# Performance work log

Measured on AMD Instinct MI355X. Metric: run time of the kernel, lower is better.

Reference implementation:

```python
import jax, jax.numpy as jnp
from jax import lax
import numpy as np

B, T, C, HID, H, W = 8, 24, 3, 32, 64, 64


def setup_inputs() -> dict:
    key = jax.random.key(0)
    ks = jax.random.split(key, 8)
    def n(k, shape, s=0.05):
        return jax.random.normal(k, shape, dtype=jnp.float32) * s
    return {
        "x": n(ks[0], (B, T, C, H, W), 1.0),
        # encoder layer 0: conv over concat(x, h) -> 4*HID gate channels
        "Wenc0": n(ks[1], (4 * HID, C + HID, 3, 3)),
        "benc0": jnp.zeros((4 * HID,), jnp.float32),
        # encoder layer 1: input is layer-0 hidden seq (HID channels)
        "Wenc1": n(ks[2], (4 * HID, HID + HID, 3, 3)),
        "benc1": jnp.zeros((4 * HID,), jnp.float32),
        # decoder (1 layer, input_dim channels in)
        "Wdec": n(ks[3], (4 * HID, C + HID, 3, 3)),
        "bdec": jnp.zeros((4 * HID,), jnp.float32),
        # MLP head: HID*H*W -> 256 -> 97
        "fc1_w": n(ks[4], (256, HID * H * W), 0.01),
        "fc1_b": jnp.zeros((256,), jnp.float32),
        "fc2_w": n(ks[5], (97, 256)),
        "fc2_b": jnp.zeros((97,), jnp.float32),
    }


def _cell_step(h, c, x_t, Wk, b):
    # ConvLSTM cell: conv(concat(x,h)) -> i,f,o,g gates
    z = lax.conv_general_dilated(
        jnp.concatenate([x_t, h], axis=1), Wk,
        window_strides=(1, 1), padding='SAME',
        dimension_numbers=('NCHW', 'OIHW', 'NCHW')) + b[None, :, None, None]
    i, f, o, g = jnp.split(z, 4, axis=1)
    c_new = jax.nn.sigmoid(f) * c + jax.nn.sigmoid(i) * jnp.tanh(g)
    h_new = jax.nn.sigmoid(o) * jnp.tanh(c_new)
    return h_new, c_new


def _run_layer(x_tb, Wk, b):
    # x_tb: [T, B, Cin, H, W]; zero-initialized state
    h0 = jnp.zeros((x_tb.shape[1], HID, H, W), x_tb.dtype)
    c0 = jnp.zeros_like(h0)
    def step(hc, xt):
        h, c = _cell_step(hc[0], hc[1], xt, Wk, b)
        return (h, c), h
    (hT, cT), hs = lax.scan(step, (h0, c0), x_tb)
    return hs, (hT, cT)


def reference(x, Wenc0, benc0, Wenc1, benc1, Wdec, bdec, fc1_w, fc1_b, fc2_w, fc2_b):
    x_tb = jnp.transpose(x, (1, 0, 2, 3, 4))          # [T,B,C,H,W]
    hs0, _ = _run_layer(x_tb, Wenc0, benc0)           # layer-0 hidden seq
    _, (hT, cT) = _run_layer(hs0, Wenc1, benc1)       # last-layer final state
    # decoder: one step on last input frame, seeded with encoder state
    h_dec, _ = _cell_step(hT, cT, x[:, -1], Wdec, bdec)  # [B,HID,H,W]
    feat = h_dec.reshape(h_dec.shape[0], -1)          # [B, HID*H*W]
    hdn = jax.nn.relu(feat @ fc1_w.T + fc1_b)
    return hdn @ fc2_w.T + fc2_b                      # [B, 97]
```

## Files before the change

kernel.cpp:

```cpp
#include <hip/hip_runtime.h>

typedef __attribute__((ext_vector_type(8))) short short8v;
typedef __attribute__((ext_vector_type(4))) float f32x4;
typedef __attribute__((ext_vector_type(4))) unsigned int uint4v;
typedef unsigned short u16;

__device__ __forceinline__ u16 f2bf(float f) {
  unsigned u = __float_as_uint(f);
  u += 0x7FFFu + ((u >> 16) & 1u);
  return (u16)(u >> 16);
}
__device__ __forceinline__ short8v ld8(const u16* p) {
  return *reinterpret_cast<const short8v*>(p);
}
__device__ __forceinline__ float frcp(float x) { return __builtin_amdgcn_rcpf(x); }

__device__ __forceinline__ void st_cg(u16* p, uint4v v) {
  asm volatile("global_store_dwordx4 %0, %1, off sc0 sc1" :: "v"(p), "v"(v) : "memory");
}
__device__ __forceinline__ void ld2_cg(const u16* a0, const u16* a1,
                                       uint4v& v0, uint4v& v1) {
  asm volatile(
      "global_load_dwordx4 %0, %2, off sc0 sc1\n\t"
      "global_load_dwordx4 %1, %3, off sc0 sc1\n\t"
      "s_waitcnt vmcnt(0)"
      : "=&v"(v0), "=&v"(v1) : "v"(a0), "v"(a1) : "memory");
}
__device__ __forceinline__ void ld4_cg(const u16* a0, const u16* a1, const u16* a2,
                                       const u16* a3, uint4v& v0, uint4v& v1,
                                       uint4v& v2, uint4v& v3) {
  asm volatile(
      "global_load_dwordx4 %0, %4, off sc0 sc1\n\t"
      "global_load_dwordx4 %1, %5, off sc0 sc1\n\t"
      "global_load_dwordx4 %2, %6, off sc0 sc1\n\t"
      "global_load_dwordx4 %3, %7, off sc0 sc1\n\t"
      "s_waitcnt vmcnt(0)"
      : "=&v"(v0), "=&v"(v1), "=&v"(v2), "=&v"(v3)
      : "v"(a0), "v"(a1), "v"(a2), "v"(a3)
      : "memory");
}

__device__ __forceinline__ void poll_lane(const unsigned* a, unsigned tgt, bool active) {
  bool pending = active;
  while (__ballot(pending)) {
    if (pending &&
        __hip_atomic_load((unsigned*)a, __ATOMIC_RELAXED, __HIP_MEMORY_SCOPE_AGENT) >= tgt)
      pending = false;
    if (__ballot(pending)) __builtin_amdgcn_s_sleep(1);
  }
}
__device__ __forceinline__ void publish(unsigned* f, unsigned v) {
  __syncthreads();
  if (threadIdx.x == 0)
    __hip_atomic_store(f, v, __ATOMIC_RELAXED, __HIP_MEMORY_SCOPE_AGENT);
}

__global__ void k_pack(const float* __restrict__ We0, const float* __restrict__ We1,
                       const float* __restrict__ Wd,
                       u16* __restrict__ Wh0p, u16* __restrict__ Wx1p,
                       u16* __restrict__ Wh1p, u16* __restrict__ Whdp,
                       u16* __restrict__ Wx0p, u16* __restrict__ Wxdp,
                       unsigned* __restrict__ flags) {
  int i = blockIdx.x * 256 + threadIdx.x;
  if (i < 8192) flags[i] = 0u;
  if (i < 147456) {
    int tbl = i / 36864, j = i % 36864;
    int s = j >> 12, cg = (j >> 11) & 1, gate = (j >> 9) & 3,
        chl = (j >> 5) & 15, ci = j & 31;
    int co = gate * 32 + cg * 16 + chl;
    float v;
    if (tbl == 0)      v = We0[(co * 35 + 3 + ci) * 9 + s];
    else if (tbl == 1) v = We1[(co * 64 + ci) * 9 + s];
    else if (tbl == 2) v = We1[(co * 64 + 32 + ci) * 9 + s];
    else               v = Wd[(co * 35 + 3 + ci) * 9 + s];
    u16* dst = tbl == 0 ? Wh0p : tbl == 1 ? Wx1p : tbl == 2 ? Wh1p : Whdp;
    dst[j] = f2bf(v);
  } else {
    int j = i - 147456, tbl = j >> 12;
    j &= 4095;
    int cg = (j >> 11) & 1, gate = (j >> 9) & 3, chl = (j >> 5) & 15, k = j & 31;
    int co = gate * 32 + cg * 16 + chl;
    const float* src = tbl ? Wd : We0;
    u16 v = (k < 27) ? f2bf(src[(co * 35 + (k % 3)) * 9 + (k / 3)]) : (u16)0;
    (tbl ? Wxdp : Wx0p)[j] = v;
  }
}

__global__ void k_im2col(const float* __restrict__ x, u16* __restrict__ out) {
  int p = blockIdx.x * 256 + threadIdx.x;
  int t = p >> 15;
  int rem = p & 32767;
  int b = rem >> 12;
  int yy = (rem >> 6) & 63;
  int xx = rem & 63;
  __align__(16) u16 buf[32];
#pragma unroll
  for (int k = 27; k < 32; k++) buf[k] = 0;
  const float* xb = x + ((size_t)(b * 24 + t)) * 3 * 4096;
#pragma unroll
  for (int ky = 0; ky < 3; ky++) {
    int ys = yy + ky - 1;
    bool yok = (unsigned)ys < 64u;
#pragma unroll
    for (int kx = 0; kx < 3; kx++) {
      int xs = xx + kx - 1;
      bool ok = yok && ((unsigned)xs < 64u);
#pragma unroll
      for (int ci = 0; ci < 3; ci++) {
        float v = ok ? xb[(size_t)ci * 4096 + ys * 64 + xs] : 0.f;
        buf[(ky * 3 + kx) * 3 + ci] = f2bf(v);
      }
    }
  }
  uint4v* dst = (uint4v*)(out + (size_t)p * 32);
  const uint4v* s = (const uint4v*)buf;
  dst[0] = s[0]; dst[1] = s[1]; dst[2] = s[2]; dst[3] = s[3];
}

__global__ __launch_bounds__(256, 1) void k_persist(
    const u16* __restrict__ imc, u16* __restrict__ hs0G, u16* __restrict__ h1G,
    const u16* __restrict__ Wx0, const u16* __restrict__ Wh0,
    const float* __restrict__ be0,
    const u16* __restrict__ Wx1, const u16* __restrict__ Wh1,
    const float* __restrict__ be1,
    const u16* __restrict__ Wxd, const u16* __restrict__ Whd,
    const float* __restrict__ bd,
    float* __restrict__ hdec, unsigned* __restrict__ flag) {
  __shared__ __align__(16) u16 smH0[8448];
  __shared__ __align__(16) u16 smH1[8448];
  const int bid = blockIdx.x;
  const int b = bid & 7;
  const int yblk = bid >> 3;
  const int y0 = yblk << 1;
  const int fi = bid * 16;
  const int tid = threadIdx.x;
  const int l = tid & 63, w = tid >> 6, lr = l & 15, g = l >> 4;
  const int mh = w >> 1, cg = w & 1, y = y0 + mh;

  if (tid < 64) {
    int q = tid & 31;
    int rgq = q >> 1, side = q & 1;
    u16* base = (tid < 32 ? smH0 : smH1) + ((size_t)(rgq * 66 + side * 65)) * 8;
    *(uint4v*)base = (uint4v)0u;
  }

  const int ch = cg * 16 + lr;
  const float bI0 = be0[ch], bF0 = be0[32 + ch], bO0 = be0[64 + ch], bG0 = be0[96 + ch];
  const float bI1 = be1[ch], bF1 = be1[32 + ch], bO1 = be1[64 + ch], bG1 = be1[96 + ch];
  const float bId = bd[ch],  bFd = bd[32 + ch],  bOd = bd[64 + ch],  bGd = bd[96 + ch];
  float c0r[16], c1r[16];
#pragma unroll
  for (int i = 0; i < 16; i++) { c0r[i] = 0.f; c1r[i] = 0.f; }

  const int pxs = tid >> 2, gqs = tid & 3;
  const size_t rbG = (size_t)b * 131072;
  const size_t poff = (size_t)pxs * 32 + gqs * 8;
  const int rup = (yblk == 0) ? y0 : y0 - 1;
  const int rdn = (yblk == 31) ? y0 + 1 : y0 + 2;
  u16* dUp0 = smH0 + ((size_t)(gqs * 66 + pxs + 1)) * 8;
  u16* dDn0 = smH0 + ((size_t)((12 + gqs) * 66 + pxs + 1)) * 8;
  u16* dUp1 = smH1 + ((size_t)(gqs * 66 + pxs + 1)) * 8;
  u16* dDn1 = smH1 + ((size_t)((12 + gqs) * 66 + pxs + 1)) * 8;

  auto do_shifts = [&](const u16* sm, const u16* __restrict__ W, f32x4 (&acc)[4][4]) {
#pragma unroll
    for (int sft = 0; sft < 9; sft++) {
      const int ky = sft / 3, dx = sft % 3 - 1;
      const u16* wb = W + ((size_t)(sft * 2 + cg) * 64 + lr) * 32 + g * 8;
      short8v B0 = ld8(wb), B1 = ld8(wb + 512), B2 = ld8(wb + 1024), B3 = ld8(wb + 1536);
      const u16* abase = sm + ((size_t)(((mh + ky) * 4 + g) * 66 + lr + dx + 1)) * 8;
#pragma unroll
      for (int mt = 0; mt < 4; mt++) {
        short8v A = ld8(abase + mt * 128);
        acc[mt][0] = __builtin_amdgcn_mfma_f32_16x16x32_bf16(A, B0, acc[mt][0], 0, 0, 0);
        acc[mt][1] = __builtin_amdgcn_mfma_f32_16x16x32_bf16(A, B1, acc[mt][1], 0, 0, 0);
        acc[mt][2] = __builtin_amdgcn_mfma_f32_16x16x32_bf16(A, B2, acc[mt][2], 0, 0, 0);
        acc[mt][3] = __builtin_amdgcn_mfma_f32_16x16x32_bf16(A, B3, acc[mt][3], 0, 0, 0);
      }
    }
  };
  auto imcol = [&](const u16* xp, const u16* __restrict__ W, f32x4 (&acc)[4][4]) {
    const u16* ab = xp + rbG + (size_t)y * 2048 + g * 8;
    const u16* wb = W + (cg * 64 + lr) * 32 + g * 8;
    short8v B0 = ld8(wb), B1 = ld8(wb + 512), B2 = ld8(wb + 1024), B3 = ld8(wb + 1536);
#pragma unroll
    for (int mt = 0; mt < 4; mt++) {
      short8v A = ld8(ab + (mt * 16 + lr) * 32);
      acc[mt][0] = __builtin_amdgcn_mfma_f32_16x16x32_bf16(A, B0, acc[mt][0], 0, 0, 0);
      acc[mt][1] = __builtin_amdgcn_mfma_f32_16x16x32_bf16(A, B1, acc[mt][1], 0, 0, 0);
      acc[mt][2] = __builtin_amdgcn_mfma_f32_16x16x32_bf16(A, B2, acc[mt][2], 0, 0, 0);
      acc[mt][3] = __builtin_amdgcn_mfma_f32_16x16x32_bf16(A, B3, acc[mt][3], 0, 0, 0);
    }
  };
  auto gates = [&](f32x4 (&acc)[4][4], float* cr, float bI, float bF, float bO,
                   float bG, u16* hbf) {
#pragma unroll
    for (int mt = 0; mt < 4; mt++) {
#pragma unroll
      for (int j = 0; j < 4; j++) {
        float zi = acc[mt][0][j] + bI, zf = acc[mt][1][j] + bF;
        float zo = acc[mt][2][j] + bO, zg = acc[mt][3][j] + bG;
        float ei = __expf(-zi), ef = __expf(-zf), eo = __expf(-zo);
        float eg = __expf(2.f * zg);
        float cn = frcp(1.f + ef) * cr[mt * 4 + j] +
                   (eg - 1.f) * frcp((1.f + ei) * (eg + 1.f));
        float ec = __expf(2.f * cn);
        cr[mt * 4 + j] = cn;
        hbf[mt * 4 + j] = f2bf((ec - 1.f) * frcp((1.f + eo) * (ec + 1.f)));
      }
    }
  };

  for (int s = 0; s <= 25; ++s) {
    if (s > 0 && tid < 64) {
      const unsigned* a = nullptr; bool act = false;
      if (l == 0 && yblk > 0)  { a = flag + fi - 128; act = true; }
      if (l == 1 && yblk < 31) { a = flag + fi + 128; act = true; }
      poll_lane(a, (unsigned)s, act);
    }
    __syncthreads();

    const bool st0 = (s >= 1 && s <= 24);
    const bool st1 = (s >= 2);
    if (st0 || st1) {
      const u16* h0src = hs0G + (size_t)((s - 1) & 1) * 1048576 + rbG;
      const u16* h1src = h1G + (size_t)(s & 1) * 1048576 + rbG;
      uint4v v0 = (uint4v)0u, v1 = (uint4v)0u, v2 = (uint4v)0u, v3 = (uint4v)0u;
      if (st0 && st1)
        ld4_cg(h0src + (size_t)rup * 2048 + poff, h0src + (size_t)rdn * 2048 + poff,
               h1src + (size_t)rup * 2048 + poff, h1src + (size_t)rdn * 2048 + poff,
               v0, v1, v2, v3);
      else if (st0)
        ld2_cg(h0src + (size_t)rup * 2048 + poff, h0src + (size_t)rdn * 2048 + poff,
               v0, v1);
      else
        ld2_cg(h1src + (size_t)rup * 2048 + poff, h1src + (size_t)rdn * 2048 + poff,
               v2, v3);
      if (yblk == 0)  { v0 = (uint4v)0u; v2 = (uint4v)0u; }
      if (yblk == 31) { v1 = (uint4v)0u; v3 = (uint4v)0u; }
      if (st0) { *(uint4v*)dUp0 = v0; *(uint4v*)dDn0 = v1; }
      if (st1) { *(uint4v*)dUp1 = v2; *(uint4v*)dDn1 = v3; }
    }
    __syncthreads();

    const bool doL0 = (s <= 23);
    const bool doL1 = (s >= 1 && s <= 24);
    u16 hbf0[16], hbf1[16];

    if (doL0) {
      f32x4 acc[4][4];
#pragma unroll
      for (int i = 0; i < 4; i++)
#pragma unroll
        for (int j = 0; j < 4; j++) acc[i][j] = (f32x4)0.f;
      imcol(imc + (size_t)s * 1048576, Wx0, acc);
      if (s >= 1) do_shifts(smH0, Wh0, acc);
      gates(acc, c0r, bI0, bF0, bO0, bG0, hbf0);
    }
    if (doL1) {
      f32x4 acc[4][4];
#pragma unroll
      for (int i = 0; i < 4; i++)
#pragma unroll
        for (int j = 0; j < 4; j++) acc[i][j] = (f32x4)0.f;
      do_shifts(smH0, Wx1, acc);
      if (s >= 2) do_shifts(smH1, Wh1, acc);
      gates(acc, c1r, bI1, bF1, bO1, bG1, hbf1);
    }
    if (s == 25) {
      f32x4 acc[4][4];
#pragma unroll
      for (int i = 0; i < 4; i++)
#pragma unroll
        for (int j = 0; j < 4; j++) acc[i][j] = (f32x4)0.f;
      imcol(imc + (size_t)23 * 1048576, Wxd, acc);
      do_shifts(smH1, Whd, acc);
#pragma unroll
      for (int mt = 0; mt < 4; mt++) {
#pragma unroll
        for (int j = 0; j < 4; j++) {
          int px = mt * 16 + g * 4 + j;
          float zi = acc[mt][0][j] + bId, zf = acc[mt][1][j] + bFd;
          float zo = acc[mt][2][j] + bOd, zg = acc[mt][3][j] + bGd;
          float ei = __expf(-zi), ef = __expf(-zf), eo = __expf(-zo);
          float eg = __expf(2.f * zg);
          float cn = frcp(1.f + ef) * c1r[mt * 4 + j] +
                     (eg - 1.f) * frcp((1.f + ei) * (eg + 1.f));
          float ec = __expf(2.f * cn);
          float hn = (ec - 1.f) * frcp((1.f + eo) * (ec + 1.f));
          hdec[((size_t)(b * 32 + ch) * 64 + y) * 64 + px] = hn;
        }
      }
      return;
    }
    __syncthreads();

    if (doL0) {
#pragma unroll
      for (int mt = 0; mt < 4; mt++)
#pragma unroll
        for (int j = 0; j < 4; j++) {
          int px = mt * 16 + g * 4 + j;
          smH0[((size_t)((1 + mh) * 4 + (ch >> 3)) * 66 + px + 1) * 8 + (ch & 7)] =
              hbf0[mt * 4 + j];
        }
    }
    if (doL1) {
#pragma unroll
      for (int mt = 0; mt < 4; mt++)
#pragma unroll
        for (int j = 0; j < 4; j++) {
          int px = mt * 16 + g * 4 + j;
          smH1[((size_t)((1 + mh) * 4 + (ch >> 3)) * 66 + px + 1) * 8 + (ch & 7)] =
              hbf1[mt * 4 + j];
        }
    }
    __syncthreads();

    if (doL0) {
      u16* d = hs0G + (size_t)(s & 1) * 1048576 + rbG;
      st_cg(d + (size_t)y0 * 2048 + poff,
            *(const uint4v*)(smH0 + ((size_t)(4 + gqs) * 66 + pxs + 1) * 8));
      st_cg(d + (size_t)(y0 + 1) * 2048 + poff,
            *(const uint4v*)(smH0 + ((size_t)(8 + gqs) * 66 + pxs + 1) * 8));
    }
    if (doL1) {
      u16* d = h1G + (size_t)((s - 1) & 1) * 1048576 + rbG;
      st_cg(d + (size_t)y0 * 2048 + poff,
            *(const uint4v*)(smH1 + ((size_t)(4 + gqs) * 66 + pxs + 1) * 8));
      st_cg(d + (size_t)(y0 + 1) * 2048 + poff,
            *(const uint4v*)(smH1 + ((size_t)(8 + gqs) * 66 + pxs + 1) * 8));
    }
    publish(flag + fi, (unsigned)(s + 1));
  }
}

__global__ __launch_bounds__(256) void k_fc1(const float* __restrict__ w,
                                             const float* __restrict__ feat,
                                             float* __restrict__ partial) {
  __shared__ float fsm[8][1024];
  const int ng = blockIdx.x, ks = blockIdx.y;
  const int tid = threadIdx.x;
  const float* fb = feat + (size_t)ks * 1024;
  for (int i = tid; i < 2048; i += 256) {
    int bb = i >> 8, kk = (i & 255) << 2;
    *(f32x4*)&fsm[bb][kk] = *(const f32x4*)(fb + (size_t)bb * 131072 + kk);
  }
  __syncthreads();
  const int wv = tid >> 6, lane = tid & 63;
  const int n0 = ng * 16 + wv * 4;
  const float* wr = w + (size_t)n0 * 131072 + (size_t)ks * 1024;
  float acc[4][8];
#pragma unroll
  for (int i = 0; i < 4; i++)
#pragma unroll
    for (int j = 0; j < 8; j++) acc[i][j] = 0.f;
#pragma unroll
  for (int it = 0; it < 4; it++) {
    int k = it * 256 + lane * 4;
    f32x4 w0 = *(const f32x4*)(wr + k);
    f32x4 w1 = *(const f32x4*)(wr + 131072 + k);
    f32x4 w2 = *(const f32x4*)(wr + 262144 + k);
    f32x4 w3 = *(const f32x4*)(wr + 393216 + k);
#pragma unroll
    for (int bb = 0; bb < 8; bb++) {
      f32x4 fv = *(const f32x4*)&fsm[bb][k];
      acc[0][bb] += w0[0] * fv[0] + w0[1] * fv[1] + w0[2] * fv[2] + w0[3] * fv[3];
      acc[1][bb] += w1[0] * fv[0] + w1[1] * fv[1] + w1[2] * fv[2] + w1[3] * fv[3];
      acc[2][bb] += w2[0] * fv[0] + w2[1] * fv[1] + w2[2] * fv[2] + w2[3] * fv[3];
      acc[3][bb] += w3[0] * fv[0] + w3[1] * fv[1] + w3[2] * fv[2] + w3[3] * fv[3];
    }
  }
#pragma unroll
  for (int nn = 0; nn < 4; nn++)
#pragma unroll
    for (int bb = 0; bb < 8; bb++) {
      float v = acc[nn][bb];
#pragma unroll
      for (int m = 32; m >= 1; m >>= 1) v += __shfl_xor(v, m, 64);
      if (lane == 0) partial[((size_t)ks * 8 + bb) * 256 + n0 + nn] = v;
    }
}

__global__ void k_fc1_fin(const float* __restrict__ partial,
                          const float* __restrict__ b1, float* __restrict__ hdn) {
  int i = blockIdx.x * 256 + threadIdx.x;
  if (i >= 2048) return;
  int b = i >> 8, n = i & 255;
  float v = b1[n];
  for (int ks = 0; ks < 128; ks++) v += partial[((size_t)ks * 8 + b) * 256 + n];
  hdn[i] = fmaxf(v, 0.f);
}

__global__ void k_fc2(const float* __restrict__ hdn, const float* __restrict__ w2,
                      const float* __restrict__ b2, float* __restrict__ out) {
  int i = blockIdx.x * 256 + threadIdx.x;
  if (i >= 776) return;
  int b = i / 97, m = i % 97;
  const float* h = hdn + b * 256;
  const float* wr = w2 + m * 256;
  float v = b2[m];
  for (int k = 0; k < 256; k++) v += h[k] * wr[k];
  out[i] = v;
}

extern "C" void kernel_launch(void* const* d_in, const int* in_sizes, int n_in,
                              void* d_out, int out_size, void* d_ws, size_t ws_size,
                              hipStream_t stream) {
  const float* x   = (const float*)d_in[0];
  const float* We0 = (const float*)d_in[1];
  const float* be0 = (const float*)d_in[2];
  const float* We1 = (const float*)d_in[3];
  const float* be1 = (const float*)d_in[4];
  const float* Wd  = (const float*)d_in[5];
  const float* bd  = (const float*)d_in[6];
  const float* f1w = (const float*)d_in[7];
  const float* f1b = (const float*)d_in[8];
  const float* f2w = (const float*)d_in[9];
  const float* f2b = (const float*)d_in[10];

  char* ws = (char*)d_ws;
  u16*      imc  = (u16*)(ws + 0);
  u16*      hs0G = (u16*)(ws + 50331648);
  u16*      h1G  = (u16*)(ws + 54525952);
  u16*      wp   = (u16*)(ws + 58720256);
  float*    hdec = (float*)(ws + 62914560);
  unsigned* flag = (unsigned*)(ws + 67108864);
  float*    part = (float*)(ws + 0);
  float*    hdn  = (float*)(ws + 1048576);
  u16 *Wh0p = wp, *Wx1p = wp + 36864, *Wh1p = wp + 73728, *Whdp = wp + 110592,
      *Wx0p = wp + 147456, *Wxdp = wp + 151552;

  k_pack<<<608, 256, 0, stream>>>(We0, We1, Wd, Wh0p, Wx1p, Wh1p, Whdp, Wx0p,
                                  Wxdp, flag);
  k_im2col<<<3072, 256, 0, stream>>>(x, imc);

  k_persist<<<256, 256, 0, stream>>>(imc, hs0G, h1G, Wx0p, Wh0p, be0,
                                     Wx1p, Wh1p, be1, Wxdp, Whdp, bd, hdec, flag);

  k_fc1<<<dim3(16, 128), 256, 0, stream>>>(f1w, hdec, part);
  k_fc1_fin<<<8, 256, 0, stream>>>(part, f1b, hdn);
  k_fc2<<<4, 256, 0, stream>>>(hdn, f2w, f2b, (float*)d_out);
}
```

Measured before the change: 375.4 us.

## Split layer-0 and layer-1 work across separate wave groups in persistent kernel

The persistent ConvLSTM kernel goes from 256 to 512 threads per block. Waves 0-3 compute encoder layer 0 and waves 4-7 compute layer 1, where before the same waves ran both layers one after the other. Each half also loads and stores its own halo rows, and each thread keeps a single cell-state array. This is meant to run the two layers' MFMA work concurrently and reduce per-thread register pressure, at the cost of larger blocks and an extra barrier per step.

```diff
diff --git a/kernel.cpp b/kernel.cpp
--- a/kernel.cpp
+++ b/kernel.cpp
@@ -25,19 +25,6 @@
       "global_load_dwordx4 %1, %3, off sc0 sc1\n\t"
       "s_waitcnt vmcnt(0)"
       : "=&v"(v0), "=&v"(v1) : "v"(a0), "v"(a1) : "memory");
-}
-__device__ __forceinline__ void ld4_cg(const u16* a0, const u16* a1, const u16* a2,
-                                       const u16* a3, uint4v& v0, uint4v& v1,
-                                       uint4v& v2, uint4v& v3) {
-  asm volatile(
-      "global_load_dwordx4 %0, %4, off sc0 sc1\n\t"
-      "global_load_dwordx4 %1, %5, off sc0 sc1\n\t"
-      "global_load_dwordx4 %2, %6, off sc0 sc1\n\t"
-      "global_load_dwordx4 %3, %7, off sc0 sc1\n\t"
-      "s_waitcnt vmcnt(0)"
-      : "=&v"(v0), "=&v"(v1), "=&v"(v2), "=&v"(v3)
-      : "v"(a0), "v"(a1), "v"(a2), "v"(a3)
-      : "memory");
 }
 
 __device__ __forceinline__ void poll_lane(const unsigned* a, unsigned tgt, bool active) {
@@ -117,7 +104,7 @@
   dst[0] = s[0]; dst[1] = s[1]; dst[2] = s[2]; dst[3] = s[3];
 }
 
-__global__ __launch_bounds__(256, 1) void k_persist(
+__global__ __launch_bounds__(512, 1) void k_persist(
     const u16* __restrict__ imc, u16* __restrict__ hs0G, u16* __restrict__ h1G,
     const u16* __restrict__ Wx0, const u16* __restrict__ Wh0,
     const float* __restrict__ be0,
@@ -134,8 +121,10 @@
   const int y0 = yblk << 1;
   const int fi = bid * 16;
   const int tid = threadIdx.x;
-  const int l = tid & 63, w = tid >> 6, lr = l & 15, g = l >> 4;
-  const int mh = w >> 1, cg = w & 1, y = y0 + mh;
+  const int w = tid >> 6, l = tid & 63, lr = l & 15, g = l >> 4;
+  const bool isL1w = w >= 4;
+  const int lw = w & 3, mh = lw >> 1, cg = lw & 1, y = y0 + mh;
+  const int ch = cg * 16 + lr;
 
   if (tid < 64) {
     int q = tid & 31;
@@ -144,23 +133,22 @@
     *(uint4v*)base = (uint4v)0u;
   }
 
-  const int ch = cg * 16 + lr;
-  const float bI0 = be0[ch], bF0 = be0[32 + ch], bO0 = be0[64 + ch], bG0 = be0[96 + ch];
-  const float bI1 = be1[ch], bF1 = be1[32 + ch], bO1 = be1[64 + ch], bG1 = be1[96 + ch];
-  const float bId = bd[ch],  bFd = bd[32 + ch],  bOd = bd[64 + ch],  bGd = bd[96 + ch];
-  float c0r[16], c1r[16];
-#pragma unroll
-  for (int i = 0; i < 16; i++) { c0r[i] = 0.f; c1r[i] = 0.f; }
-
-  const int pxs = tid >> 2, gqs = tid & 3;
+  const float* bia = isL1w ? be1 : be0;
+  const float bI = bia[ch], bF = bia[32 + ch], bO = bia[64 + ch], bG = bia[96 + ch];
+  float cr[16];
+#pragma unroll
+  for (int i = 0; i < 16; i++) cr[i] = 0.f;
+
+  const int sthr = tid & 255;
+  const int sgrp = tid >> 8;
+  const int pxs = sthr >> 2, gqs = sthr & 3;
   const size_t rbG = (size_t)b * 131072;
   const size_t poff = (size_t)pxs * 32 + gqs * 8;
   const int rup = (yblk == 0) ? y0 : y0 - 1;
   const int rdn = (yblk == 31) ? y0 + 1 : y0 + 2;
-  u16* dUp0 = smH0 + ((size_t)(gqs * 66 + pxs + 1)) * 8;
-  u16* dDn0 = smH0 + ((size_t)((12 + gqs) * 66 + pxs + 1)) * 8;
-  u16* dUp1 = smH1 + ((size_t)(gqs * 66 + pxs + 1)) * 8;
-  u16* dDn1 = smH1 + ((size_t)((12 + gqs) * 66 + pxs + 1)) * 8;
+  u16* smS = sgrp ? smH1 : smH0;
+  u16* dUp = smS + ((size_t)(gqs * 66 + pxs + 1)) * 8;
+  u16* dDn = smS + ((size_t)((12 + gqs) * 66 + pxs + 1)) * 8;
 
   auto do_shifts = [&](const u16* sm, const u16* __restrict__ W, f32x4 (&acc)[4][4]) {
 #pragma unroll
@@ -192,8 +180,7 @@
       acc[mt][3] = __builtin_amdgcn_mfma_f32_16x16x32_bf16(A, B3, acc[mt][3], 0, 0, 0);
     }
   };
-  auto gates = [&](f32x4 (&acc)[4][4], float* cr, float bI, float bF, float bO,
-                   float bG, u16* hbf) {
+  auto gates = [&](f32x4 (&acc)[4][4], u16* hbf) {
 #pragma unroll
     for (int mt = 0; mt < 4; mt++) {
 #pragma unroll
@@ -220,32 +207,57 @@
     }
     __syncthreads();
 
-    const bool st0 = (s >= 1 && s <= 24);
-    const bool st1 = (s >= 2);
-    if (st0 || st1) {
-      const u16* h0src = hs0G + (size_t)((s - 1) & 1) * 1048576 + rbG;
-      const u16* h1src = h1G + (size_t)(s & 1) * 1048576 + rbG;
-      uint4v v0 = (uint4v)0u, v1 = (uint4v)0u, v2 = (uint4v)0u, v3 = (uint4v)0u;
-      if (st0 && st1)
-        ld4_cg(h0src + (size_t)rup * 2048 + poff, h0src + (size_t)rdn * 2048 + poff,
-               h1src + (size_t)rup * 2048 + poff, h1src + (size_t)rdn * 2048 + poff,
-               v0, v1, v2, v3);
-      else if (st0)
-        ld2_cg(h0src + (size_t)rup * 2048 + poff, h0src + (size_t)rdn * 2048 + poff,
-               v0, v1);
-      else
-        ld2_cg(h1src + (size_t)rup * 2048 + poff, h1src + (size_t)rdn * 2048 + poff,
-               v2, v3);
-      if (yblk == 0)  { v0 = (uint4v)0u; v2 = (uint4v)0u; }
-      if (yblk == 31) { v1 = (uint4v)0u; v3 = (uint4v)0u; }
-      if (st0) { *(uint4v*)dUp0 = v0; *(uint4v*)dDn0 = v1; }
-      if (st1) { *(uint4v*)dUp1 = v2; *(uint4v*)dDn1 = v3; }
+    if (sgrp == 0 && s >= 1 && s <= 24) {
+      const u16* src = hs0G + (size_t)((s - 1) & 1) * 1048576 + rbG;
+      uint4v v0, v1;
+      ld2_cg(src + (size_t)rup * 2048 + poff, src + (size_t)rdn * 2048 + poff, v0, v1);
+      if (yblk == 0)  v0 = (uint4v)0u;
+      if (yblk == 31) v1 = (uint4v)0u;
+      *(uint4v*)dUp = v0; *(uint4v*)dDn = v1;
+    }
+    if (sgrp == 1 && s >= 2) {
+      const u16* src = h1G + (size_t)(s & 1) * 1048576 + rbG;
+      uint4v v0, v1;
+      ld2_cg(src + (size_t)rup * 2048 + poff, src + (size_t)rdn * 2048 + poff, v0, v1);
+      if (yblk == 0)  v0 = (uint4v)0u;
+      if (yblk == 31) v1 = (uint4v)0u;
+      *(uint4v*)dUp = v0; *(uint4v*)dDn = v1;
     }
     __syncthreads();
 
-    const bool doL0 = (s <= 23);
-    const bool doL1 = (s >= 1 && s <= 24);
-    u16 hbf0[16], hbf1[16];
+    if (s == 25) {
+      if (isL1w) {
+        f32x4 acc[4][4];
+#pragma unroll
+        for (int i = 0; i < 4; i++)
+#pragma unroll
+          for (int j = 0; j < 4; j++) acc[i][j] = (f32x4)0.f;
+        imcol(imc + (size_t)23 * 1048576, Wxd, acc);
+        do_shifts(smH1, Whd, acc);
+        const float bId = bd[ch], bFd = bd[32 + ch], bOd = bd[64 + ch], bGd = bd[96 + ch];
+#pragma unroll
+        for (int mt = 0; mt < 4; mt++) {
+#pragma unroll
+          for (int j = 0; j < 4; j++) {
+            int px = mt * 16 + g * 4 + j;
+            float zi = acc[mt][0][j] + bId, zf = acc[mt][1][j] + bFd;
+            float zo = acc[mt][2][j] + bOd, zg = acc[mt][3][j] + bGd;
+            float ei = __expf(-zi), ef = __expf(-zf), eo = __expf(-zo);
+            float eg = __expf(2.f * zg);
+            float cn = frcp(1.f + ef) * cr[mt * 4 + j] +
+                       (eg - 1.f) * frcp((1.f + ei) * (eg + 1.f));
+            float ec = __expf(2.f * cn);
+            float hn = (ec - 1.f) * frcp((1.f + eo) * (ec + 1.f));
+            hdec[((size_t)(b * 32 + ch) * 64 + y) * 64 + px] = hn;
+          }
+        }
+      }
+      return;
+    }
+
+    const bool doL0 = !isL1w && s <= 23;
+    const bool doL1 = isL1w && s >= 1 && s <= 24;
+    u16 hbf[16];
 
     if (doL0) {
       f32x4 acc[4][4];
@@ -255,7 +267,7 @@
         for (int j = 0; j < 4; j++) acc[i][j] = (f32x4)0.f;
       imcol(imc + (size_t)s * 1048576, Wx0, acc);
       if (s >= 1) do_shifts(smH0, Wh0, acc);
-      gates(acc, c0r, bI0, bF0, bO0, bG0, hbf0);
+      gates(acc, hbf);
     }
     if (doL1) {
       f32x4 acc[4][4];
@@ -265,66 +277,31 @@
         for (int j = 0; j < 4; j++) acc[i][j] = (f32x4)0.f;
       do_shifts(smH0, Wx1, acc);
       if (s >= 2) do_shifts(smH1, Wh1, acc);
-      gates(acc, c1r, bI1, bF1, bO1, bG1, hbf1);
-    }
-    if (s == 25) {
-      f32x4 acc[4][4];
-#pragma unroll
-      for (int i = 0; i < 4; i++)
-#pragma unroll
-        for (int j = 0; j < 4; j++) acc[i][j] = (f32x4)0.f;
-      imcol(imc + (size_t)23 * 1048576, Wxd, acc);
-      do_shifts(smH1, Whd, acc);
-#pragma unroll
-      for (int mt = 0; mt < 4; mt++) {
+      gates(acc, hbf);
+    }
+    __syncthreads();
+
+    if (doL0 || doL1) {
+      u16* smD = isL1w ? smH1 : smH0;
+#pragma unroll
+      for (int mt = 0; mt < 4; mt++)
 #pragma unroll
         for (int j = 0; j < 4; j++) {
           int px = mt * 16 + g * 4 + j;
-          float zi = acc[mt][0][j] + bId, zf = acc[mt][1][j] + bFd;
-          float zo = acc[mt][2][j] + bOd, zg = acc[mt][3][j] + bGd;
-          float ei = __expf(-zi), ef = __expf(-zf), eo = __expf(-zo);
-          float eg = __expf(2.f * zg);
-          float cn = frcp(1.f + ef) * c1r[mt * 4 + j] +
-                     (eg - 1.f) * frcp((1.f + ei) * (eg + 1.f));
-          float ec = __expf(2.f * cn);
-          float hn = (ec - 1.f) * frcp((1.f + eo) * (ec + 1.f));
-          hdec[((size_t)(b * 32 + ch) * 64 + y) * 64 + px] = hn;
+          smD[((size_t)((1 + mh) * 4 + (ch >> 3)) * 66 + px + 1) * 8 + (ch & 7)] =
+              hbf[mt * 4 + j];
         }
-      }
-      return;
     }
     __syncthreads();
 
-    if (doL0) {
-#pragma unroll
-      for (int mt = 0; mt < 4; mt++)
-#pragma unroll
-        for (int j = 0; j < 4; j++) {
-          int px = mt * 16 + g * 4 + j;
-          smH0[((size_t)((1 + mh) * 4 + (ch >> 3)) * 66 + px + 1) * 8 + (ch & 7)] =
-              hbf0[mt * 4 + j];
-        }
-    }
-    if (doL1) {
-#pragma unroll
-      for (int mt = 0; mt < 4; mt++)
-#pragma unroll
-        for (int j = 0; j < 4; j++) {
-          int px = mt * 16 + g * 4 + j;
-          smH1[((size_t)((1 + mh) * 4 + (ch >> 3)) * 66 + px + 1) * 8 + (ch & 7)] =
-              hbf1[mt * 4 + j];
-        }
-    }
-    __syncthreads();
-
-    if (doL0) {
+    if (sgrp == 0 && s <= 23) {
       u16* d = hs0G + (size_t)(s & 1) * 1048576 + rbG;
       st_cg(d + (size_t)y0 * 2048 + poff,
             *(const uint4v*)(smH0 + ((size_t)(4 + gqs) * 66 + pxs + 1) * 8));
       st_cg(d + (size_t)(y0 + 1) * 2048 + poff,
             *(const uint4v*)(smH0 + ((size_t)(8 + gqs) * 66 + pxs + 1) * 8));
     }
-    if (doL1) {
+    if (sgrp == 1 && s >= 1 && s <= 24) {
       u16* d = h1G + (size_t)((s - 1) & 1) * 1048576 + rbG;
       st_cg(d + (size_t)y0 * 2048 + poff,
             *(const uint4v*)(smH1 + ((size_t)(4 + gqs) * 66 + pxs + 1) * 8));
@@ -435,7 +412,7 @@
                                   Wxdp, flag);
   k_im2col<<<3072, 256, 0, stream>>>(x, imc);
 
-  k_persist<<<256, 256, 0, stream>>>(imc, hs0G, h1G, Wx0p, Wh0p, be0,
+  k_persist<<<256, 512, 0, stream>>>(imc, hs0G, h1G, Wx0p, Wh0p, be0,
                                      Wx1p, Wh1p, be1, Wxdp, Whdp, bd, hdec, flag);
 
   k_fc1<<<dim3(16, 128), 256, 0, stream>>>(f1w, hdec, part);
```

Result: faster. 337.1 us (-10.2%).

## Split persistent ConvLSTM into one-row blocks with layer-specialized waves

Applied to the files above, without the earlier changes.

The persistent recurrent kernel now launches 512 blocks of one image row each instead of 256 blocks of two rows. Within a block, waves 0-1 compute encoder layer 0 and waves 2-3 compute layer 1 (and the decoder step), where before every wave ran both layers in sequence. Launch bounds now request two blocks per CU. The goal is to shorten the serial per-timestep critical path and raise occupancy, at the cost of twice as many neighbour-flag syncs and halo loads, and an uneven load between the layer-0 and layer-1 waves.

```diff
diff --git a/kernel.cpp b/kernel.cpp
--- a/kernel.cpp
+++ b/kernel.cpp
@@ -117,7 +117,7 @@
   dst[0] = s[0]; dst[1] = s[1]; dst[2] = s[2]; dst[3] = s[3];
 }
 
-__global__ __launch_bounds__(256, 1) void k_persist(
+__global__ __launch_bounds__(256, 2) void k_persist(
     const u16* __restrict__ imc, u16* __restrict__ hs0G, u16* __restrict__ h1G,
     const u16* __restrict__ Wx0, const u16* __restrict__ Wh0,
     const float* __restrict__ be0,
@@ -126,41 +126,41 @@
     const u16* __restrict__ Wxd, const u16* __restrict__ Whd,
     const float* __restrict__ bd,
     float* __restrict__ hdec, unsigned* __restrict__ flag) {
-  __shared__ __align__(16) u16 smH0[8448];
-  __shared__ __align__(16) u16 smH1[8448];
+  __shared__ __align__(16) u16 smH0[6336];
+  __shared__ __align__(16) u16 smH1[6336];
   const int bid = blockIdx.x;
   const int b = bid & 7;
   const int yblk = bid >> 3;
-  const int y0 = yblk << 1;
+  const int y0 = yblk;
   const int fi = bid * 16;
   const int tid = threadIdx.x;
-  const int l = tid & 63, w = tid >> 6, lr = l & 15, g = l >> 4;
-  const int mh = w >> 1, cg = w & 1, y = y0 + mh;
-
-  if (tid < 64) {
-    int q = tid & 31;
+  const int w = tid >> 6, l = tid & 63, lr = l & 15, g = l >> 4;
+  const bool isL1w = w >= 2;
+  const int cg = w & 1;
+  const int ch = cg * 16 + lr;
+
+  if (tid < 48) {
+    int op = tid / 24, q = tid % 24;
     int rgq = q >> 1, side = q & 1;
-    u16* base = (tid < 32 ? smH0 : smH1) + ((size_t)(rgq * 66 + side * 65)) * 8;
+    u16* base = (op ? smH1 : smH0) + ((size_t)(rgq * 66 + side * 65)) * 8;
     *(uint4v*)base = (uint4v)0u;
   }
 
-  const int ch = cg * 16 + lr;
-  const float bI0 = be0[ch], bF0 = be0[32 + ch], bO0 = be0[64 + ch], bG0 = be0[96 + ch];
-  const float bI1 = be1[ch], bF1 = be1[32 + ch], bO1 = be1[64 + ch], bG1 = be1[96 + ch];
-  const float bId = bd[ch],  bFd = bd[32 + ch],  bOd = bd[64 + ch],  bGd = bd[96 + ch];
-  float c0r[16], c1r[16];
-#pragma unroll
-  for (int i = 0; i < 16; i++) { c0r[i] = 0.f; c1r[i] = 0.f; }
+  const float* bia = isL1w ? be1 : be0;
+  const float bI = bia[ch], bF = bia[32 + ch], bO = bia[64 + ch], bG = bia[96 + ch];
+  float cr[16];
+#pragma unroll
+  for (int i = 0; i < 16; i++) cr[i] = 0.f;
 
   const int pxs = tid >> 2, gqs = tid & 3;
   const size_t rbG = (size_t)b * 131072;
   const size_t poff = (size_t)pxs * 32 + gqs * 8;
   const int rup = (yblk == 0) ? y0 : y0 - 1;
-  const int rdn = (yblk == 31) ? y0 + 1 : y0 + 2;
+  const int rdn = (yblk == 63) ? y0 : y0 + 1;
   u16* dUp0 = smH0 + ((size_t)(gqs * 66 + pxs + 1)) * 8;
-  u16* dDn0 = smH0 + ((size_t)((12 + gqs) * 66 + pxs + 1)) * 8;
+  u16* dDn0 = smH0 + ((size_t)((8 + gqs) * 66 + pxs + 1)) * 8;
   u16* dUp1 = smH1 + ((size_t)(gqs * 66 + pxs + 1)) * 8;
-  u16* dDn1 = smH1 + ((size_t)((12 + gqs) * 66 + pxs + 1)) * 8;
+  u16* dDn1 = smH1 + ((size_t)((8 + gqs) * 66 + pxs + 1)) * 8;
 
   auto do_shifts = [&](const u16* sm, const u16* __restrict__ W, f32x4 (&acc)[4][4]) {
 #pragma unroll
@@ -168,7 +168,7 @@
       const int ky = sft / 3, dx = sft % 3 - 1;
       const u16* wb = W + ((size_t)(sft * 2 + cg) * 64 + lr) * 32 + g * 8;
       short8v B0 = ld8(wb), B1 = ld8(wb + 512), B2 = ld8(wb + 1024), B3 = ld8(wb + 1536);
-      const u16* abase = sm + ((size_t)(((mh + ky) * 4 + g) * 66 + lr + dx + 1)) * 8;
+      const u16* abase = sm + ((size_t)((ky * 4 + g) * 66 + lr + dx + 1)) * 8;
 #pragma unroll
       for (int mt = 0; mt < 4; mt++) {
         short8v A = ld8(abase + mt * 128);
@@ -180,7 +180,7 @@
     }
   };
   auto imcol = [&](const u16* xp, const u16* __restrict__ W, f32x4 (&acc)[4][4]) {
-    const u16* ab = xp + rbG + (size_t)y * 2048 + g * 8;
+    const u16* ab = xp + rbG + (size_t)y0 * 2048 + g * 8;
     const u16* wb = W + (cg * 64 + lr) * 32 + g * 8;
     short8v B0 = ld8(wb), B1 = ld8(wb + 512), B2 = ld8(wb + 1024), B3 = ld8(wb + 1536);
 #pragma unroll
@@ -192,8 +192,7 @@
       acc[mt][3] = __builtin_amdgcn_mfma_f32_16x16x32_bf16(A, B3, acc[mt][3], 0, 0, 0);
     }
   };
-  auto gates = [&](f32x4 (&acc)[4][4], float* cr, float bI, float bF, float bO,
-                   float bG, u16* hbf) {
+  auto gates = [&](f32x4 (&acc)[4][4], u16* hbf) {
 #pragma unroll
     for (int mt = 0; mt < 4; mt++) {
 #pragma unroll
@@ -215,7 +214,7 @@
     if (s > 0 && tid < 64) {
       const unsigned* a = nullptr; bool act = false;
       if (l == 0 && yblk > 0)  { a = flag + fi - 128; act = true; }
-      if (l == 1 && yblk < 31) { a = flag + fi + 128; act = true; }
+      if (l == 1 && yblk < 63) { a = flag + fi + 128; act = true; }
       poll_lane(a, (unsigned)s, act);
     }
     __syncthreads();
@@ -237,15 +236,45 @@
         ld2_cg(h1src + (size_t)rup * 2048 + poff, h1src + (size_t)rdn * 2048 + poff,
                v2, v3);
       if (yblk == 0)  { v0 = (uint4v)0u; v2 = (uint4v)0u; }
-      if (yblk == 31) { v1 = (uint4v)0u; v3 = (uint4v)0u; }
+      if (yblk == 63) { v1 = (uint4v)0u; v3 = (uint4v)0u; }
       if (st0) { *(uint4v*)dUp0 = v0; *(uint4v*)dDn0 = v1; }
       if (st1) { *(uint4v*)dUp1 = v2; *(uint4v*)dDn1 = v3; }
     }
     __syncthreads();
 
-    const bool doL0 = (s <= 23);
-    const bool doL1 = (s >= 1 && s <= 24);
-    u16 hbf0[16], hbf1[16];
+    if (s == 25) {
+      if (isL1w) {
+        f32x4 acc[4][4];
+#pragma unroll
+        for (int i = 0; i < 4; i++)
+#pragma unroll
+          for (int j = 0; j < 4; j++) acc[i][j] = (f32x4)0.f;
+        imcol(imc + (size_t)23 * 1048576, Wxd, acc);
+        do_shifts(smH1, Whd, acc);
+        const float bId = bd[ch], bFd = bd[32 + ch], bOd = bd[64 + ch], bGd = bd[96 + ch];
+#pragma unroll
+        for (int mt = 0; mt < 4; mt++) {
+#pragma unroll
+          for (int j = 0; j < 4; j++) {
+            int px = mt * 16 + g * 4 + j;
+            float zi = acc[mt][0][j] + bId, zf = acc[mt][1][j] + bFd;
+            float zo = acc[mt][2][j] + bOd, zg = acc[mt][3][j] + bGd;
+            float ei = __expf(-zi), ef = __expf(-zf), eo = __expf(-zo);
+            float eg = __expf(2.f * zg);
+            float cn = frcp(1.f + ef) * cr[mt * 4 + j] +
+                       (eg - 1.f) * frcp((1.f + ei) * (eg + 1.f));
+            float ec = __expf(2.f * cn);
+            float hn = (ec - 1.f) * frcp((1.f + eo) * (ec + 1.f));
+            hdec[((size_t)(b * 32 + ch) * 64 + y0) * 64 + px] = hn;
+          }
+        }
+      }
+      return;
+    }
+
+    const bool doL0 = !isL1w && s <= 23;
+    const bool doL1 = isL1w && s >= 1 && s <= 24;
+    u16 hbf[16];
 
     if (doL0) {
       f32x4 acc[4][4];
@@ -255,7 +284,7 @@
         for (int j = 0; j < 4; j++) acc[i][j] = (f32x4)0.f;
       imcol(imc + (size_t)s * 1048576, Wx0, acc);
       if (s >= 1) do_shifts(smH0, Wh0, acc);
-      gates(acc, c0r, bI0, bF0, bO0, bG0, hbf0);
+      gates(acc, hbf);
     }
     if (doL1) {
       f32x4 acc[4][4];
@@ -265,71 +294,32 @@
         for (int j = 0; j < 4; j++) acc[i][j] = (f32x4)0.f;
       do_shifts(smH0, Wx1, acc);
       if (s >= 2) do_shifts(smH1, Wh1, acc);
-      gates(acc, c1r, bI1, bF1, bO1, bG1, hbf1);
-    }
-    if (s == 25) {
-      f32x4 acc[4][4];
-#pragma unroll
-      for (int i = 0; i < 4; i++)
-#pragma unroll
-        for (int j = 0; j < 4; j++) acc[i][j] = (f32x4)0.f;
-      imcol(imc + (size_t)23 * 1048576, Wxd, acc);
-      do_shifts(smH1, Whd, acc);
-#pragma unroll
-      for (int mt = 0; mt < 4; mt++) {
+      gates(acc, hbf);
+    }
+    __syncthreads();
+
+    if (doL0 || doL1) {
+      u16* smD = isL1w ? smH1 : smH0;
+      const int gq = ch >> 3;
+#pragma unroll
+      for (int mt = 0; mt < 4; mt++)
 #pragma unroll
         for (int j = 0; j < 4; j++) {
           int px = mt * 16 + g * 4 + j;
-          float zi = acc[mt][0][j] + bId, zf = acc[mt][1][j] + bFd;
-          float zo = acc[mt][2][j] + bOd, zg = acc[mt][3][j] + bGd;
-          float ei = __expf(-zi), ef = __expf(-zf), eo = __expf(-zo);
-          float eg = __expf(2.f * zg);
-          float cn = frcp(1.f + ef) * c1r[mt * 4 + j] +
-                     (eg - 1.f) * frcp((1.f + ei) * (eg + 1.f));
-          float ec = __expf(2.f * cn);
-          float hn = (ec - 1.f) * frcp((1.f + eo) * (ec + 1.f));
-          hdec[((size_t)(b * 32 + ch) * 64 + y) * 64 + px] = hn;
+          smD[((size_t)((4 + gq) * 66 + px + 1)) * 8 + (ch & 7)] = hbf[mt * 4 + j];
         }
-      }
-      return;
     }
     __syncthreads();
 
-    if (doL0) {
-#pragma unroll
-      for (int mt = 0; mt < 4; mt++)
-#pragma unroll
-        for (int j = 0; j < 4; j++) {
-          int px = mt * 16 + g * 4 + j;
-          smH0[((size_t)((1 + mh) * 4 + (ch >> 3)) * 66 + px + 1) * 8 + (ch & 7)] =
-              hbf0[mt * 4 + j];
-        }
-    }
-    if (doL1) {
-#pragma unroll
-      for (int mt = 0; mt < 4; mt++)
-#pragma unroll
-        for (int j = 0; j < 4; j++) {
-          int px = mt * 16 + g * 4 + j;
-          smH1[((size_t)((1 + mh) * 4 + (ch >> 3)) * 66 + px + 1) * 8 + (ch & 7)] =
-              hbf1[mt * 4 + j];
-        }
-    }
-    __syncthreads();
-
-    if (doL0) {
+    if (s <= 23) {
       u16* d = hs0G + (size_t)(s & 1) * 1048576 + rbG;
       st_cg(d + (size_t)y0 * 2048 + poff,
-            *(const uint4v*)(smH0 + ((size_t)(4 + gqs) * 66 + pxs + 1) * 8));
-      st_cg(d + (size_t)(y0 + 1) * 2048 + poff,
-            *(const uint4v*)(smH0 + ((size_t)(8 + gqs) * 66 + pxs + 1) * 8));
-    }
-    if (doL1) {
+            *(const uint4v*)(smH0 + ((size_t)((4 + gqs) * 66 + pxs + 1)) * 8));
+    }
+    if (s >= 1 && s <= 24) {
       u16* d = h1G + (size_t)((s - 1) & 1) * 1048576 + rbG;
       st_cg(d + (size_t)y0 * 2048 + poff,
-            *(const uint4v*)(smH1 + ((size_t)(4 + gqs) * 66 + pxs + 1) * 8));
-      st_cg(d + (size_t)(y0 + 1) * 2048 + poff,
-            *(const uint4v*)(smH1 + ((size_t)(8 + gqs) * 66 + pxs + 1) * 8));
+            *(const uint4v*)(smH1 + ((size_t)((4 + gqs) * 66 + pxs + 1)) * 8));
     }
     publish(flag + fi, (unsigned)(s + 1));
   }
@@ -435,7 +425,7 @@
                                   Wxdp, flag);
   k_im2col<<<3072, 256, 0, stream>>>(x, imc);
 
-  k_persist<<<256, 256, 0, stream>>>(imc, hs0G, h1G, Wx0p, Wh0p, be0,
+  k_persist<<<512, 256, 0, stream>>>(imc, hs0G, h1G, Wx0p, Wh0p, be0,
                                      Wx1p, Wh1p, be1, Wxdp, Whdp, bd, hdec, flag);
 
   k_fc1<<<dim3(16, 128), 256, 0, stream>>>(f1w, hdec, part);
```

Result: faster. 349.5 us (-6.9%).
